# Optimization experiments

Measured on AMD Instinct MI355X. Metric: run time of the kernel, lower is better.

The kernel has to match this reference:

```python
import jax, jax.numpy as jnp
import numpy as np

B, TE, T = 256, 300, 600
NIN, NPV, H, EMB, NS, NHE = 128, 5, 512, 32, 4, 16
SCALE = 1.0 / float(np.sqrt(H))


def gru_cell(h, x, Wih, Whh, bih, bhh):
    # PyTorch GRU cell: r,z,n gate ordering
    gi = x @ Wih.T + bih
    gh = h @ Whh.T + bhh
    i_r, i_z, i_n = jnp.split(gi, 3, axis=-1)
    h_r, h_z, h_n = jnp.split(gh, 3, axis=-1)
    r = jax.nn.sigmoid(i_r + h_r)
    z = jax.nn.sigmoid(i_z + h_z)
    n = jnp.tanh(i_n + r * h_n)
    return (1.0 - z) * n + z * h


def setup_inputs():
    key = jax.random.key(0)
    ks = iter(jax.random.split(key, 40))
    w = lambda shape: jax.random.normal(next(ks), shape, jnp.float32) * SCALE
    inp = {
        'x_cv': jax.random.normal(next(ks), (B, TE, NIN), jnp.float32),
        'x_cv_target': jax.random.normal(next(ks), (B, T, NIN), jnp.float32),
        'pv_init': jax.random.normal(next(ks), (B, NPV), jnp.float32),
        'scenario': jax.random.randint(next(ks), (B,), 0, NS),
        'emb': w((NS, EMB)),
        'enc_Wih0': w((3 * H, NIN + EMB)), 'enc_Whh0': w((3 * H, H)), 'enc_bih0': w((3 * H,)), 'enc_bhh0': w((3 * H,)),
        'enc_Wih1': w((3 * H, H)), 'enc_Whh1': w((3 * H, H)), 'enc_bih1': w((3 * H,)), 'enc_bhh1': w((3 * H,)),
        'dec_Wih0': w((3 * H, NIN + NPV)), 'dec_Whh0': w((3 * H, H)), 'dec_bih0': w((3 * H,)), 'dec_bhh0': w((3 * H,)),
        'dec_Wih1': w((3 * H, H)), 'dec_Whh1': w((3 * H, H)), 'dec_bih1': w((3 * H,)), 'dec_bhh1': w((3 * H,)),
        'fc1_W': w((128, H)), 'fc1_b': w((128,)), 'fc2_W': w((NPV, 128)), 'fc2_b': w((NPV,)),
        'he1_W': w((128, H)), 'he1_b': w((128,)), 'he2_W': w((NHE, 128)), 'he2_b': w((NHE,)),
    }
    return inp


def _forward(x_cv, x_cv_target, pv_init, scenario, emb, enc_Wih0, enc_Whh0, enc_bih0, enc_bhh0, enc_Wih1, enc_Whh1, enc_bih1, enc_bhh1, dec_Wih0, dec_Whh0, dec_bih0, dec_bhh0, dec_Wih1, dec_Whh1, dec_bih1, dec_bhh1, fc1_W, fc1_b, fc2_W, fc2_b, he1_W, he1_b, he2_W, he2_b):
    Bb = x_cv.shape[0]
    Hh = enc_Whh0.shape[1]
    emb_s = emb[scenario]  # (B, EMB)
    enc_in = jnp.concatenate([x_cv, jnp.broadcast_to(emb_s[:, None, :], (Bb, x_cv.shape[1], emb.shape[1]))], axis=-1)
    x_t = jnp.swapaxes(enc_in, 0, 1)  # (TE, B, NIN+EMB)
    h0 = jnp.zeros((Bb, Hh), enc_in.dtype)

    def step0(h, xt):
        hn = gru_cell(h, xt, enc_Wih0, enc_Whh0, enc_bih0, enc_bhh0)
        return hn, hn
    h1_fin, seq1 = jax.lax.scan(step0, h0, x_t)

    def step1(h, xt):
        hn = gru_cell(h, xt, enc_Wih1, enc_Whh1, enc_bih1, enc_bhh1)
        return hn, hn
    h2_fin, _ = jax.lax.scan(step1, h0, seq1)

    xt_tgt = jnp.swapaxes(x_cv_target, 0, 1)  # (T, B, NIN)

    def dec_step(carry, xt):
        d1, d2, pv = carry
        inp = jnp.concatenate([xt, pv], axis=-1)
        d1 = gru_cell(d1, inp, dec_Wih0, dec_Whh0, dec_bih0, dec_bhh0)
        d2 = gru_cell(d2, d1, dec_Wih1, dec_Whh1, dec_bih1, dec_bhh1)
        pv_new = jnp.maximum(d2 @ fc1_W.T + fc1_b, 0.0) @ fc2_W.T + fc2_b
        he_new = jnp.maximum(d2 @ he1_W.T + he1_b, 0.0) @ he2_W.T + he2_b
        return (d1, d2, pv_new), (pv_new, he_new)

    _, (pv_seq, he_seq) = jax.lax.scan(dec_step, (h1_fin, h2_fin, pv_init), xt_tgt)
    pv_out = jnp.swapaxes(pv_seq, 0, 1)  # (B, T, NPV)
    he_out = jnp.swapaxes(he_seq, 0, 1)  # (B, T, NHE)
    return pv_out, he_out


def reference(x_cv, x_cv_target, pv_init, scenario, emb, enc_Wih0, enc_Whh0, enc_bih0, enc_bhh0, enc_Wih1, enc_Whh1, enc_bih1, enc_bhh1, dec_Wih0, dec_Whh0, dec_bih0, dec_bhh0, dec_Wih1, dec_Whh1, dec_bih1, dec_bhh1, fc1_W, fc1_b, fc2_W, fc2_b, he1_W, he1_b, he2_W, he2_b):
    return _forward(x_cv, x_cv_target, pv_init, scenario, emb, enc_Wih0, enc_Whh0, enc_bih0, enc_bhh0, enc_Wih1, enc_Whh1, enc_bih1, enc_bhh1, dec_Wih0, dec_Whh0, dec_bih0, dec_bhh0, dec_Wih1, dec_Whh1, dec_bih1, dec_bhh1, fc1_W, fc1_b, fc2_W, fc2_b, he1_W, he1_b, he2_W, he2_b)
```

## Files before the change

kernel.cpp:

```cpp
#include <hip/hip_runtime.h>

#define NTHR 512
#define NBLK 256

#define B_    256
#define TE_   300
#define T_    600
#define NIN_  128
#define H_    512
#define EMB_  32
#define KE0_  160
#define KD0_  136
#define OUT_HE_OFS 768000ull

#define ACT_F (32 * 68)
#define W_F   (48 * 68)

constexpr size_t OF_BAR  = 0;
constexpr size_t OF_XEMB = 1024;
constexpr size_t OF_HA   = OF_XEMB + 8192;
constexpr size_t OF_HB   = OF_HA + 262144;
constexpr size_t OF_PV   = OF_HB + 262144;
constexpr size_t OF_S1   = OF_PV + 2048;
constexpr size_t OF_S2   = OF_S1 + 32768;
constexpr size_t OF_E0I  = OF_S2 + 32768;
constexpr size_t OF_E0H  = OF_E0I + 245760;
constexpr size_t OF_E1I  = OF_E0H + 786432;
constexpr size_t OF_E1H  = OF_E1I + 786432;
constexpr size_t OF_D0I  = OF_E1H + 786432;
constexpr size_t OF_D0H  = OF_D0I + 208896;
constexpr size_t OF_D1I  = OF_D0H + 786432;
constexpr size_t OF_D1H  = OF_D1I + 786432;
constexpr size_t OF_FH   = OF_D1H + 786432;
constexpr size_t WS_END  = OF_FH + 131072;

__global__ void k_init(float* __restrict__ ws, const float* __restrict__ pv_init,
                       const int* __restrict__ scen, const float* __restrict__ emb) {
  const size_t total = 1024 + 8192 + 2048 + 131072 + 131072;
  size_t stride = (size_t)gridDim.x * blockDim.x;
  for (size_t x = (size_t)blockIdx.x * blockDim.x + threadIdx.x; x < total; x += stride) {
    if (x < 1024) {
      ((unsigned*)ws)[x] = 0u;
    } else if (x < 1024 + 8192) {
      size_t r = x - 1024; int b = (int)(r >> 5), e = (int)(r & 31);
      ws[OF_XEMB + r] = emb[scen[b] * EMB_ + e];
    } else if (x < 1024 + 8192 + 2048) {
      size_t r = x - 1024 - 8192; int b = (int)(r >> 3), p = (int)(r & 7);
      ws[OF_PV + r] = (p < 5) ? pv_init[b * 5 + p] : 0.f;
    } else if (x < 1024 + 8192 + 2048 + 131072) {
      ws[OF_HA + 131072 + (x - 1024 - 8192 - 2048)] = 0.f;
    } else {
      ws[OF_HB + 131072 + (x - 1024 - 8192 - 2048 - 131072)] = 0.f;
    }
  }
}

__global__ void k_rearr(float* __restrict__ dst, const float* __restrict__ src, int K, int Kp) {
  int n = 32 * 48 * Kp;
  for (int idx = blockIdx.x * blockDim.x + threadIdx.x; idx < n; idx += gridDim.x * blockDim.x) {
    int g = idx / (48 * Kp), r = idx % (48 * Kp), c = r / Kp, k = r % Kp;
    int j = (c >> 4) * 512 + g * 16 + (c & 15);
    dst[idx] = (k < K) ? src[j * K + k] : 0.f;
  }
}
__global__ void k_rearr_fh(float* __restrict__ dst, const float* __restrict__ fc1,
                           const float* __restrict__ he1) {
  int n = 32 * 8 * 512;
  for (int idx = blockIdx.x * blockDim.x + threadIdx.x; idx < n; idx += gridDim.x * blockDim.x) {
    int g = idx / (8 * 512), r = idx % (8 * 512), c = r / 512, k = r % 512;
    const float* s = (c < 4) ? fc1 : he1;
    dst[idx] = s[(g * 4 + (c & 3)) * 512 + k];
  }
}

__device__ __forceinline__ float sigm(float x) { return 1.f / (1.f + __expf(-x)); }
__device__ __forceinline__ float tanhx(float x) { float e = __expf(2.f * x); return 1.f - 2.f / (e + 1.f); }

__device__ __forceinline__ void bar_sync_bi(unsigned* bar, int big) {
  __syncthreads();
  if (threadIdx.x == 0) {
    unsigned* cnt = &bar[big << 6];
    unsigned* gen = &bar[(big << 6) + 16];
    unsigned g0 = __hip_atomic_load(gen, __ATOMIC_RELAXED, __HIP_MEMORY_SCOPE_AGENT);
    unsigned n = __hip_atomic_fetch_add(cnt, 1u, __ATOMIC_ACQ_REL, __HIP_MEMORY_SCOPE_AGENT);
    if (n == 31u) {
      __hip_atomic_store(cnt, 0u, __ATOMIC_RELAXED, __HIP_MEMORY_SCOPE_AGENT);
      __hip_atomic_store(gen, g0 + 1u, __ATOMIC_RELEASE, __HIP_MEMORY_SCOPE_AGENT);
    } else {
      while (__hip_atomic_load(gen, __ATOMIC_ACQUIRE, __HIP_MEMORY_SCOPE_AGENT) == g0)
        __builtin_amdgcn_s_sleep(1);
    }
  }
  __syncthreads();
}

#define FMA4(ACC, AV, WV)                                   \
  ACC = fmaf(AV.x, WV.x, ACC); ACC = fmaf(AV.y, WV.y, ACC); \
  ACC = fmaf(AV.z, WV.z, ACC); ACC = fmaf(AV.w, WV.w, ACC);

#define GQ4(Q, AX)                                                                   \
  { const int q_ = (Q);                                                              \
    const float4 wr = W4c[hc * 17 + q_];                                             \
    const float4 wz = W4c[(16 + hc) * 17 + q_];                                      \
    const float4 wn = W4c[(32 + hc) * 17 + q_];                                      \
    const float4 a0 = A4c[(rb + 0) * 17 + q_];                                       \
    const float4 a1 = A4c[(rb + 1) * 17 + q_];                                       \
    const float4 a2 = A4c[(rb + 2) * 17 + q_];                                       \
    const float4 a3 = A4c[(rb + 3) * 17 + q_];                                       \
    FMA4(aR[0], a0, wr) FMA4(aR[1], a1, wr) FMA4(aR[2], a2, wr) FMA4(aR[3], a3, wr)  \
    FMA4(aZ[0], a0, wz) FMA4(aZ[1], a1, wz) FMA4(aZ[2], a2, wz) FMA4(aZ[3], a3, wz)  \
    FMA4(AX[0], a0, wn) FMA4(AX[1], a1, wn) FMA4(AX[2], a2, wn) FMA4(AX[3], a3, wn)  \
  }

template <int KIND, int KI>
__device__ __forceinline__ void stage_pref(
    int kt, int tid, int b0, int g, int t,
    const float* __restrict__ actA, const float* __restrict__ actB,
    const float* __restrict__ wi, const float* __restrict__ wh,
    const float* __restrict__ hprev,
    float4& wv0, float4& wv1, float4& av, bool& w0v, bool& w1v, bool& a_v) {
  constexpr int NTI = (KI + 63) >> 6;
  w0v = false; w1v = false; a_v = false;
  if (kt < NTI) {
    const int k0 = kt << 6;
    const int cnt = (KI - k0 >= 64) ? 64 : (KI - k0);
    const int L = (cnt == 64) ? 4 : (cnt == 32) ? 3 : 1;
    const int M = (1 << L) - 1;
    if (tid < (48 << L)) {
      w0v = true;
      const int c0 = tid >> L, f0 = tid & M;
      wv0 = *(const float4*)(wi + (size_t)(g * 48 + c0) * KI + k0 + (f0 << 2));
    }
    const int i1 = tid + 512;
    if (i1 < (48 << L)) {
      w1v = true;
      const int c1 = i1 >> L, f1 = i1 & M;
      wv1 = *(const float4*)(wi + (size_t)(g * 48 + c1) * KI + k0 + (f1 << 2));
    }
    if (tid < (32 << L)) {
      const int row = tid >> L, f = tid & M;
      if (KIND == 1) {
        av = *(const float4*)(actA + (size_t)(b0 + row) * H_ + k0 + (f << 2)); a_v = true;
      } else if (KIND == 0) {
        if (k0 < 128) {
          av = *(const float4*)(actA + ((size_t)(b0 + row) * TE_ + t) * NIN_ + k0 + (f << 2)); a_v = true;
        } else {
          av = *(const float4*)(actB + (size_t)(b0 + row) * EMB_ + (f << 2)); a_v = true;
        }
      } else {
        if (k0 < 128) {
          av = *(const float4*)(actA + ((size_t)(b0 + row) * T_ + t) * NIN_ + k0 + (f << 2)); a_v = true;
        }
      }
    }
  } else {
    const int k0 = (kt - NTI) << 6;
    w0v = true;
    wv0 = *(const float4*)(wh + (size_t)(g * 48 + (tid >> 4)) * 512 + k0 + ((tid & 15) << 2));
    if (tid < 256) {
      w1v = true;
      wv1 = *(const float4*)(wh + (size_t)(g * 48 + 32 + (tid >> 4)) * 512 + k0 + ((tid & 15) << 2));
    }
    av = *(const float4*)(hprev + (size_t)(b0 + (tid >> 4)) * H_ + k0 + ((tid & 15) << 2));
    a_v = true;
  }
}

template <int KIND, int KI>
__device__ __forceinline__ void stage_write(
    int kt, int tid, float* __restrict__ s_act_b, float* __restrict__ s_w_b,
    const float4& wv0, const float4& wv1, const float4& av,
    bool w0v, bool w1v, bool a_v, const float* __restrict__ s_pvl) {
  constexpr int NTI = (KI + 63) >> 6;
  const bool is_input = (kt < NTI);
  const int k0i = kt << 6;
  const int cnt = is_input ? ((KI - k0i >= 64) ? 64 : (KI - k0i)) : 64;
  const int L = (cnt == 64) ? 4 : (cnt == 32) ? 3 : 1;
  const int M = (1 << L) - 1;
  float4* W4 = (float4*)s_w_b;
  float4* A4 = (float4*)s_act_b;
  if (w0v) W4[(tid >> L) * 17 + (tid & M)] = wv0;
  if (w1v) { const int i1 = tid + 512; W4[(i1 >> L) * 17 + (i1 & M)] = wv1; }
  if (a_v) A4[(tid >> L) * 17 + (tid & M)] = av;
  if (KIND == 2 && is_input && k0i == 128 && tid < 64) {
    const int row = tid >> 1, f = tid & 1;
    float4 v;
    if (f == 0) {
      v.x = s_pvl[(row << 3) + 0]; v.y = s_pvl[(row << 3) + 1];
      v.z = s_pvl[(row << 3) + 2]; v.w = s_pvl[(row << 3) + 3];
    } else {
      v.x = s_pvl[(row << 3) + 4]; v.y = 0.f; v.z = 0.f; v.w = 0.f;
    }
    A4[row * 17 + f] = v;
  }
}

template <int KIND, int KI>
__device__ void gru_tile(const float* __restrict__ actA, const float* __restrict__ actB, int t,
                         const float* __restrict__ wi, const float* __restrict__ wh,
                         const float* __restrict__ bi, const float* __restrict__ bh,
                         const float* __restrict__ hprev, float* __restrict__ hout,
                         int b0, int g, float* __restrict__ s_act, float* __restrict__ s_w,
                         float* __restrict__ s_sb, const float* __restrict__ s_pvl) {
  const int tid = threadIdx.x;
  const int hc = tid & 15;
  const int ks = (tid >> 4) & 3;
  const int rq = tid >> 6;
  const int rb = rq << 2;
  float aR[4] = {0.f,0.f,0.f,0.f}, aZ[4] = {0.f,0.f,0.f,0.f};
  float aX[4] = {0.f,0.f,0.f,0.f}, aN[4] = {0.f,0.f,0.f,0.f};
  constexpr int NTI = (KI + 63) >> 6;
  constexpr int NTT = NTI + 8;

  float4 wv0 = {0,0,0,0}, wv1 = {0,0,0,0}, av = {0,0,0,0};
  bool w0v = false, w1v = false, a_v = false;
  stage_pref<KIND, KI>(0, tid, b0, g, t, actA, actB, wi, wh, hprev, wv0, wv1, av, w0v, w1v, a_v);
  stage_write<KIND, KI>(0, tid, s_act, s_w, wv0, wv1, av, w0v, w1v, a_v, s_pvl);

  for (int kt = 0; kt < NTT; ++kt) {
    const bool is_input = (kt < NTI);
    const int k0i = kt << 6;
    const int cnt = is_input ? ((KI - k0i >= 64) ? 64 : (KI - k0i)) : 64;
    const int cur = kt & 1;

    __syncthreads();
    if (kt + 1 < NTT)
      stage_pref<KIND, KI>(kt + 1, tid, b0, g, t, actA, actB, wi, wh, hprev, wv0, wv1, av, w0v, w1v, a_v);

    const float4* A4c = (const float4*)(s_act + cur * ACT_F);
    const float4* W4c = (const float4*)(s_w + cur * W_F);
    if (is_input) {
      if (cnt == 64) {
        const int qb = ks << 2;
#pragma unroll 2
        for (int ch = 0; ch < 4; ++ch) GQ4(qb + ch, aX)
      } else if (cnt == 32) {
        const int qb = ks << 1;
#pragma unroll 2
        for (int ch = 0; ch < 2; ++ch) GQ4(qb + ch, aX)
      } else {
        if (ks < 2) GQ4(ks, aX)
      }
    } else {
      const int qb = ks << 2;
#pragma unroll 2
      for (int ch = 0; ch < 4; ++ch) GQ4(qb + ch, aN)
    }

    if (kt + 1 < NTT)
      stage_write<KIND, KI>(kt + 1, tid, s_act + (cur ^ 1) * ACT_F, s_w + (cur ^ 1) * W_F,
                            wv0, wv1, av, w0v, w1v, a_v, s_pvl);
  }

  __syncthreads();

#pragma unroll
  for (int j = 0; j < 4; ++j) {
    aR[j] += __shfl_xor(aR[j], 16); aR[j] += __shfl_xor(aR[j], 32);
    aZ[j] += __shfl_xor(aZ[j], 16); aZ[j] += __shfl_xor(aZ[j], 32);
    aX[j] += __shfl_xor(aX[j], 16); aX[j] += __shfl_xor(aX[j], 32);
    aN[j] += __shfl_xor(aN[j], 16); aN[j] += __shfl_xor(aN[j], 32);
  }

  {
    const float sR = (ks & 2) ? ((ks & 1) ? aR[3] : aR[2]) : ((ks & 1) ? aR[1] : aR[0]);
    const float sZ = (ks & 2) ? ((ks & 1) ? aZ[3] : aZ[2]) : ((ks & 1) ? aZ[1] : aZ[0]);
    const float sX = (ks & 2) ? ((ks & 1) ? aX[3] : aX[2]) : ((ks & 1) ? aX[1] : aX[0]);
    const float sN = (ks & 2) ? ((ks & 1) ? aN[3] : aN[2]) : ((ks & 1) ? aN[1] : aN[0]);
    const int hid = (g << 4) + hc;
    const int row = rb + ks;
    const float r = sigm(sR + bi[hid] + bh[hid]);
    const float z = sigm(sZ + bi[512 + hid] + bh[512 + hid]);
    const float n = tanhx(sX + bi[1024 + hid] + r * (sN + bh[1024 + hid]));
    const float hp = hprev[(size_t)(b0 + row) * H_ + hid];
    hout[(size_t)(b0 + row) * H_ + hid] = (1.f - z) * n + z * hp;
  }
}

__global__ __launch_bounds__(NTHR, 1) void k_main(
    float* __restrict__ ws, const float* __restrict__ x_cv, const float* __restrict__ x_tgt,
    const float* __restrict__ e_bi0, const float* __restrict__ e_bh0,
    const float* __restrict__ e_bi1, const float* __restrict__ e_bh1,
    const float* __restrict__ d_bi0, const float* __restrict__ d_bh0,
    const float* __restrict__ d_bi1, const float* __restrict__ d_bh1,
    const float* __restrict__ fc1_b, const float* __restrict__ fc2_W, const float* __restrict__ fc2_b,
    const float* __restrict__ he1_b, const float* __restrict__ he2_W, const float* __restrict__ he2_b,
    float* __restrict__ out) {
  __shared__ __align__(16) float s_act[2 * ACT_F];
  __shared__ __align__(16) float s_w[2 * W_F];
  __shared__ __align__(16) float s_pv[256];
  __shared__ __align__(16) float s_sb[32 * 132];

  const int tid = threadIdx.x;
  const int wg = blockIdx.x;
  const int ji = wg & 31;
  const int bi = wg >> 5;
  const int b0 = bi << 5;

  unsigned* bar = (unsigned*)ws;
  float* xemb = ws + OF_XEMB;
  float* hA[2] = {ws + OF_HA, ws + OF_HA + 131072};
  float* hB[2] = {ws + OF_HB, ws + OF_HB + 131072};
  float* pvst = ws + OF_PV;
  float* s1g = ws + OF_S1;
  float* s2g = ws + OF_S2;
  const float* wE0I = ws + OF_E0I; const float* wE0H = ws + OF_E0H;
  const float* wE1I = ws + OF_E1I; const float* wE1H = ws + OF_E1H;
  const float* wD0I = ws + OF_D0I; const float* wD0H = ws + OF_D0H;
  const float* wD1I = ws + OF_D1I; const float* wD1H = ws + OF_D1H;
  const float* wFH  = ws + OF_FH;

  for (int s = 0; s <= TE_; ++s) {
    if (s < TE_)
      gru_tile<0, KE0_>(x_cv, xemb, s, wE0I, wE0H, e_bi0, e_bh0,
                        hA[(s + 1) & 1], hA[s & 1], b0, ji, s_act, s_w, s_sb, nullptr);
    if (s >= 1)
      gru_tile<1, 512>(hA[(s + 1) & 1], nullptr, 0, wE1I, wE1H, e_bi1, e_bh1,
                       hB[s & 1], hB[(s + 1) & 1], b0, ji, s_act, s_w, s_sb, nullptr);
    bar_sync_bi(bar, bi);
  }

  for (int t = 0; t <= T_; ++t) {
    if (t == 0) {
      if (tid < 256) s_pv[tid] = pvst[(b0 << 3) + tid];
      __syncthreads();
    } else {
      {
        int row = tid >> 4, co = (tid & 15) << 3;
        float4 v0 = *(const float4*)(s1g + (size_t)(b0 + row) * 128 + co);
        float4 v1 = *(const float4*)(s1g + (size_t)(b0 + row) * 128 + co + 4);
        *(float4*)(s_sb + row * 132 + co) = v0;
        *(float4*)(s_sb + row * 132 + co + 4) = v1;
      }
      __syncthreads();
      if (tid < 160) {
        int bl2 = tid & 31, p = tid >> 5;
        float acc = fc2_b[p];
        const float4* sb4 = (const float4*)(s_sb + bl2 * 132);
        const float4* w4 = (const float4*)(fc2_W + p * 128);
#pragma unroll 8
        for (int c = 0; c < 32; ++c) {
          float4 a = sb4[c], w = w4[c];
          acc = fmaf(a.x, w.x, acc); acc = fmaf(a.y, w.y, acc);
          acc = fmaf(a.z, w.z, acc); acc = fmaf(a.w, w.w, acc);
        }
        s_pv[(bl2 << 3) + p] = acc;
      }
      __syncthreads();
      if (ji == 1 && tid < 160) {
        int bl2 = tid & 31, p = tid >> 5;
        out[((size_t)(b0 + bl2) * T_ + (t - 1)) * 5 + p] = s_pv[(bl2 << 3) + p];
      }
      if (ji == 0) {
        int row = tid >> 4, co = (tid & 15) << 3;
        float4 v0 = *(const float4*)(s2g + (size_t)(b0 + row) * 128 + co);
        float4 v1 = *(const float4*)(s2g + (size_t)(b0 + row) * 128 + co + 4);
        *(float4*)(s_sb + row * 132 + co) = v0;
        *(float4*)(s_sb + row * 132 + co + 4) = v1;
        __syncthreads();
        int bl2 = tid & 31, e = tid >> 5;
        float acc = he2_b[e];
        const float4* sb4 = (const float4*)(s_sb + bl2 * 132);
        const float4* w4 = (const float4*)(he2_W + e * 128);
#pragma unroll 8
        for (int c = 0; c < 32; ++c) {
          float4 a = sb4[c], w = w4[c];
          acc = fmaf(a.x, w.x, acc); acc = fmaf(a.y, w.y, acc);
          acc = fmaf(a.z, w.z, acc); acc = fmaf(a.w, w.w, acc);
        }
        out[OUT_HE_OFS + ((size_t)(b0 + bl2) * T_ + (t - 1)) * 16 + e] = acc;
      }
    }

    if (t < T_) {
      gru_tile<2, KD0_>(x_tgt, nullptr, t, wD0I, wD0H, d_bi0, d_bh0,
                        hA[(t + 1) & 1], hA[t & 1], b0, ji, s_act, s_w, s_sb, s_pv);
      bar_sync_bi(bar, bi);
      gru_tile<1, 512>(hA[t & 1], nullptr, 0, wD1I, wD1H, d_bi1, d_bh1,
                       hB[(t + 1) & 1], hB[t & 1], b0, ji, s_act, s_w, s_sb, nullptr);
      bar_sync_bi(bar, bi);
      {
        const float* d2 = hB[t & 1];
        const int c = tid & 7;
        const int rp2 = (tid >> 3) & 15;
        const int ks2 = tid >> 7;
        const int r0h = rp2 << 1, r1h = r0h + 1;
        float aF0 = 0.f, aF1 = 0.f;
        float4 wv = {0,0,0,0}, av;
        if (tid < 128)
          wv = *(const float4*)(wFH + (size_t)((ji << 3) + (tid >> 4)) * 512 + ((tid & 15) << 2));
        av = *(const float4*)(d2 + (size_t)(b0 + (tid >> 4)) * H_ + ((tid & 15) << 2));
        {
          float4* W4 = (float4*)s_w;
          float4* A4 = (float4*)s_act;
          if (tid < 128) W4[(tid >> 4) * 17 + (tid & 15)] = wv;
          A4[(tid >> 4) * 17 + (tid & 15)] = av;
        }
        for (int kt = 0; kt < 8; ++kt) {
          const int cur = kt & 1;
          __syncthreads();
          if (kt + 1 < 8) {
            const int k0 = (kt + 1) << 6;
            if (tid < 128)
              wv = *(const float4*)(wFH + (size_t)((ji << 3) + (tid >> 4)) * 512 + k0 + ((tid & 15) << 2));
            av = *(const float4*)(d2 + (size_t)(b0 + (tid >> 4)) * H_ + k0 + ((tid & 15) << 2));
          }
          const float4* A4c = (const float4*)(s_act + cur * ACT_F);
          const float4* W4c = (const float4*)(s_w + cur * W_F);
          const int qb = ks2 << 2;
#pragma unroll 2
          for (int ch = 0; ch < 4; ++ch) {
            const int q_ = qb + ch;
            const float4 a0 = A4c[r0h * 17 + q_];
            const float4 a1 = A4c[r1h * 17 + q_];
            const float4 w = W4c[c * 17 + q_];
            aF0 = fmaf(a0.x, w.x, aF0); aF0 = fmaf(a0.y, w.y, aF0);
            aF0 = fmaf(a0.z, w.z, aF0); aF0 = fmaf(a0.w, w.w, aF0);
            aF1 = fmaf(a1.x, w.x, aF1); aF1 = fmaf(a1.y, w.y, aF1);
            aF1 = fmaf(a1.z, w.z, aF1); aF1 = fmaf(a1.w, w.w, aF1);
          }
          if (kt + 1 < 8) {
            float4* W4 = (float4*)(s_w + (cur ^ 1) * W_F);
            float4* A4 = (float4*)(s_act + (cur ^ 1) * ACT_F);
            if (tid < 128) W4[(tid >> 4) * 17 + (tid & 15)] = wv;
            A4[(tid >> 4) * 17 + (tid & 15)] = av;
          }
        }
        if (ks2) {
          float* rbf = s_sb + (size_t)(tid & 127) * 9 + ((ks2 - 1) << 1);
          rbf[0] = aF0; rbf[1] = aF1;
        }
        __syncthreads();
        if (tid < 128) {
          const float* rbf = s_sb + (size_t)tid * 9;
          aF0 += rbf[0] + rbf[2] + rbf[4];
          aF1 += rbf[1] + rbf[3] + rbf[5];
          if (c < 4) {
            const float bb = fc1_b[(ji << 2) + c];
            s1g[(size_t)(b0 + r0h) * 128 + (ji << 2) + c] = fmaxf(aF0 + bb, 0.f);
            s1g[(size_t)(b0 + r1h) * 128 + (ji << 2) + c] = fmaxf(aF1 + bb, 0.f);
          } else {
            const float bb = he1_b[(ji << 2) + c - 4];
            s2g[(size_t)(b0 + r0h) * 128 + (ji << 2) + c - 4] = fmaxf(aF0 + bb, 0.f);
            s2g[(size_t)(b0 + r1h) * 128 + (ji << 2) + c - 4] = fmaxf(aF1 + bb, 0.f);
          }
        }
      }
      bar_sync_bi(bar, bi);
    }
  }
}

extern "C" void kernel_launch(void* const* d_in, const int* in_sizes, int n_in,
                              void* d_out, int out_size, void* d_ws, size_t ws_size,
                              hipStream_t stream) {
  float* ws = (float*)d_ws;
  const float* x_cv   = (const float*)d_in[0];
  const float* x_tgt  = (const float*)d_in[1];
  const float* pv_init= (const float*)d_in[2];
  const int*   scen   = (const int*)d_in[3];
  const float* emb    = (const float*)d_in[4];
  const float* eWih0  = (const float*)d_in[5];
  const float* eWhh0  = (const float*)d_in[6];
  const float* ebi0   = (const float*)d_in[7];
  const float* ebh0   = (const float*)d_in[8];
  const float* eWih1  = (const float*)d_in[9];
  const float* eWhh1  = (const float*)d_in[10];
  const float* ebi1   = (const float*)d_in[11];
  const float* ebh1   = (const float*)d_in[12];
  const float* dWih0  = (const float*)d_in[13];
  const float* dWhh0  = (const float*)d_in[14];
  const float* dbi0   = (const float*)d_in[15];
  const float* dbh0   = (const float*)d_in[16];
  const float* dWih1  = (const float*)d_in[17];
  const float* dWhh1  = (const float*)d_in[18];
  const float* dbi1   = (const float*)d_in[19];
  const float* dbh1   = (const float*)d_in[20];
  const float* fc1W   = (const float*)d_in[21];
  const float* fc1b   = (const float*)d_in[22];
  const float* fc2W   = (const float*)d_in[23];
  const float* fc2b   = (const float*)d_in[24];
  const float* he1W   = (const float*)d_in[25];
  const float* he1b   = (const float*)d_in[26];
  const float* he2W   = (const float*)d_in[27];
  const float* he2b   = (const float*)d_in[28];

  hipLaunchKernelGGL(k_init, dim3(512), dim3(256), 0, stream, ws, pv_init, scen, emb);
  hipLaunchKernelGGL(k_rearr, dim3(512), dim3(256), 0, stream, ws + OF_E0I, eWih0, 160, 160);
  hipLaunchKernelGGL(k_rearr, dim3(512), dim3(256), 0, stream, ws + OF_E0H, eWhh0, 512, 512);
  hipLaunchKernelGGL(k_rearr, dim3(512), dim3(256), 0, stream, ws + OF_E1I, eWih1, 512, 512);
  hipLaunchKernelGGL(k_rearr, dim3(512), dim3(256), 0, stream, ws + OF_E1H, eWhh1, 512, 512);
  hipLaunchKernelGGL(k_rearr, dim3(512), dim3(256), 0, stream, ws + OF_D0I, dWih0, 133, 136);
  hipLaunchKernelGGL(k_rearr, dim3(512), dim3(256), 0, stream, ws + OF_D0H, dWhh0, 512, 512);
  hipLaunchKernelGGL(k_rearr, dim3(512), dim3(256), 0, stream, ws + OF_D1I, dWih1, 512, 512);
  hipLaunchKernelGGL(k_rearr, dim3(512), dim3(256), 0, stream, ws + OF_D1H, dWhh1, 512, 512);
  hipLaunchKernelGGL(k_rearr_fh, dim3(256), dim3(256), 0, stream, ws + OF_FH, fc1W, he1W);

  hipLaunchKernelGGL(k_main, dim3(NBLK), dim3(NTHR), 0, stream,
                     ws, x_cv, x_tgt, ebi0, ebh0, ebi1, ebh1, dbi0, dbh0, dbi1, dbh1,
                     fc1b, fc2W, fc2b, he1b, he2W, he2b, (float*)d_out);
}
```

Before: 75.92 ms.

## Remap thread roles and replace shuffle K-reduction with shared-memory tree reduction

Reassigns thread index bits so the K-split index comes from the high bits (whole wavefronts per K slice) and row quads from the middle bits, changing how the GEMM tile's K dimension is partitioned across wavefronts. The final reduction across K slices moves from cross-lane shuffles to a two-level tree through shared memory with extra barriers. Only a quarter of the threads then compute the gate nonlinearities, four rows each, with biases loaded once. This may change LDS access patterns in the main loop and adds barriers and LDS traffic in the epilogue, while idling most threads in the gate computation.

```diff
diff --git a/kernel.cpp b/kernel.cpp
--- a/kernel.cpp
+++ b/kernel.cpp
@@ -204,8 +204,8 @@
                          float* __restrict__ s_sb, const float* __restrict__ s_pvl) {
   const int tid = threadIdx.x;
   const int hc = tid & 15;
-  const int ks = (tid >> 4) & 3;
-  const int rq = tid >> 6;
+  const int rq = (tid >> 4) & 7;
+  const int ks = tid >> 7;
   const int rb = rq << 2;
   float aR[4] = {0.f,0.f,0.f,0.f}, aZ[4] = {0.f,0.f,0.f,0.f};
   float aX[4] = {0.f,0.f,0.f,0.f}, aN[4] = {0.f,0.f,0.f,0.f};
@@ -252,28 +252,51 @@
                             wv0, wv1, av, w0v, w1v, a_v, s_pvl);
   }
 
+  float4* sb4 = (float4*)s_sb;
   __syncthreads();
-
+  if (ks >= 2) {
+    const int idx = ((ks - 2) << 7) | (tid & 127);
+    sb4[          idx] = make_float4(aR[0], aR[1], aR[2], aR[3]);
+    sb4[256  +    idx] = make_float4(aZ[0], aZ[1], aZ[2], aZ[3]);
+    sb4[512  +    idx] = make_float4(aX[0], aX[1], aX[2], aX[3]);
+    sb4[768  +    idx] = make_float4(aN[0], aN[1], aN[2], aN[3]);
+  }
+  __syncthreads();
+  if (ks < 2) {
+    const int idx = (ks << 7) | (tid & 127);
+    const float4 vr = sb4[idx], vz = sb4[256 + idx], vx = sb4[512 + idx], vn = sb4[768 + idx];
+    aR[0] += vr.x; aR[1] += vr.y; aR[2] += vr.z; aR[3] += vr.w;
+    aZ[0] += vz.x; aZ[1] += vz.y; aZ[2] += vz.z; aZ[3] += vz.w;
+    aX[0] += vx.x; aX[1] += vx.y; aX[2] += vx.z; aX[3] += vx.w;
+    aN[0] += vn.x; aN[1] += vn.y; aN[2] += vn.z; aN[3] += vn.w;
+  }
+  __syncthreads();
+  if (ks == 1) {
+    const int idx = tid & 127;
+    sb4[          idx] = make_float4(aR[0], aR[1], aR[2], aR[3]);
+    sb4[256  +    idx] = make_float4(aZ[0], aZ[1], aZ[2], aZ[3]);
+    sb4[512  +    idx] = make_float4(aX[0], aX[1], aX[2], aX[3]);
+    sb4[768  +    idx] = make_float4(aN[0], aN[1], aN[2], aN[3]);
+  }
+  __syncthreads();
+  if (ks == 0) {
+    const int idx = tid;
+    const float4 vr = sb4[idx], vz = sb4[256 + idx], vx = sb4[512 + idx], vn = sb4[768 + idx];
+    aR[0] += vr.x; aR[1] += vr.y; aR[2] += vr.z; aR[3] += vr.w;
+    aZ[0] += vz.x; aZ[1] += vz.y; aZ[2] += vz.z; aZ[3] += vz.w;
+    aX[0] += vx.x; aX[1] += vx.y; aX[2] += vx.z; aX[3] += vx.w;
+    aN[0] += vn.x; aN[1] += vn.y; aN[2] += vn.z; aN[3] += vn.w;
+    const int hid = (g << 4) + hc;
+    const float biR = bi[hid] + bh[hid];
+    const float biZ = bi[512 + hid] + bh[512 + hid];
+    const float biN = bi[1024 + hid], bhN = bh[1024 + hid];
 #pragma unroll
-  for (int j = 0; j < 4; ++j) {
-    aR[j] += __shfl_xor(aR[j], 16); aR[j] += __shfl_xor(aR[j], 32);
-    aZ[j] += __shfl_xor(aZ[j], 16); aZ[j] += __shfl_xor(aZ[j], 32);
-    aX[j] += __shfl_xor(aX[j], 16); aX[j] += __shfl_xor(aX[j], 32);
-    aN[j] += __shfl_xor(aN[j], 16); aN[j] += __shfl_xor(aN[j], 32);
-  }
-
-  {
-    const float sR = (ks & 2) ? ((ks & 1) ? aR[3] : aR[2]) : ((ks & 1) ? aR[1] : aR[0]);
-    const float sZ = (ks & 2) ? ((ks & 1) ? aZ[3] : aZ[2]) : ((ks & 1) ? aZ[1] : aZ[0]);
-    const float sX = (ks & 2) ? ((ks & 1) ? aX[3] : aX[2]) : ((ks & 1) ? aX[1] : aX[0]);
-    const float sN = (ks & 2) ? ((ks & 1) ? aN[3] : aN[2]) : ((ks & 1) ? aN[1] : aN[0]);
-    const int hid = (g << 4) + hc;
-    const int row = rb + ks;
-    const float r = sigm(sR + bi[hid] + bh[hid]);
-    const float z = sigm(sZ + bi[512 + hid] + bh[512 + hid]);
-    const float n = tanhx(sX + bi[1024 + hid] + r * (sN + bh[1024 + hid]));
-    const float hp = hprev[(size_t)(b0 + row) * H_ + hid];
-    hout[(size_t)(b0 + row) * H_ + hid] = (1.f - z) * n + z * hp;
+    for (int j = 0; j < 4; ++j) {
+      const float r = sigm(aR[j] + biR), z = sigm(aZ[j] + biZ);
+      const float n = tanhx(aX[j] + biN + r * (aN[j] + bhN));
+      const float hp = hprev[(size_t)(b0 + rb + j) * H_ + hid];
+      hout[(size_t)(b0 + rb + j) * H_ + hid] = (1.f - z) * n + z * hp;
+    }
   }
 }
 
```

New measurement: 73.10 ms. 1.04x faster.
